# Kernel tuning notes

Measured on AMD Instinct MI355X. Metric: run time of the kernel, lower is better.

The kernel has to match this reference:

```python
import jax, jax.numpy as jnp
import numpy as np

N = 100000
E = 1600000
IN = 256
H = 4
F = 64
NEG_SLOPE = 0.05


def setup_inputs() -> dict:
    key = jax.random.key(0)
    ks = jax.random.split(key, 8)
    feat = jax.random.normal(ks[0], (N, IN), dtype=jnp.float32)
    src = jax.random.randint(ks[1], (E,), 0, N, dtype=jnp.int64)
    dst = jax.random.randint(ks[2], (E,), 0, N, dtype=jnp.int64)
    W_fc = jax.random.normal(ks[3], (H * F, IN), dtype=jnp.float32) * (2.0 / np.sqrt(IN + H * F))
    attn_l = jax.random.normal(ks[4], (H, F), dtype=jnp.float32) * 0.1
    attn_r = jax.random.normal(ks[5], (H, F), dtype=jnp.float32) * 0.1
    W_res = jax.random.normal(ks[6], (H * F, IN), dtype=jnp.float32) * (2.0 / np.sqrt(IN + H * F))
    bias = jnp.zeros((H * F,), dtype=jnp.float32)
    return {"feat": feat, "src": src, "dst": dst, "W_fc": W_fc,
            "attn_l": attn_l, "attn_r": attn_r, "W_res": W_res, "bias": bias}


def _leaky_relu(x):
    return jnp.where(x > 0, x, NEG_SLOPE * x)


def reference(feat, src, dst, W_fc, attn_l, attn_r, W_res, bias):
    # project: [N, H, F]
    feat_src = (feat @ W_fc.T).reshape(N, H, F)
    # attention logits per node: el/er [N, H]
    el = jnp.einsum('nhf,hf->nh', feat_src, attn_l)
    er = jnp.einsum('nhf,hf->nh', feat_src, attn_r)
    # edge SDDMM (u_add_v) + leaky_relu: [E, H]
    e = _leaky_relu(el[src] + er[dst])
    # edge softmax grouped by destination node
    emax = jax.ops.segment_max(e, dst, num_segments=N)          # [N, H]
    emax = jnp.where(jnp.isfinite(emax), emax, 0.0)             # empty segments
    ex = jnp.exp(e - emax[dst])                                 # [E, H]
    esum = jax.ops.segment_sum(ex, dst, num_segments=N)         # [N, H]
    a = ex / jnp.maximum(esum[dst], 1e-20)                      # [E, H]
    # u_mul_e + sum aggregation (SpMM): [N, H, F]
    msgs = feat_src[src] * a[:, :, None]                        # [E, H, F]
    rst = jax.ops.segment_sum(msgs, dst, num_segments=N)
    # residual + bias
    rst = rst + (feat @ W_res.T).reshape(N, H, F)
    rst = rst + bias.reshape(1, H, F)
    return rst, a
```

## Files before the change

### kernel.cpp

```cpp
#include <hip/hip_runtime.h>

#define NNODES 100000
#define NEDGES 1600000
#define KDIM 256
#define CDIM 256
#define NHEAD 4
#define FDIM 64
#define NEG 0.05f

typedef short bf16x8 __attribute__((ext_vector_type(8)));
typedef float f32x4  __attribute__((ext_vector_type(4)));
typedef __attribute__((address_space(3))) void*       lds_vp;
typedef __attribute__((address_space(1))) const void* glb_cvp;

__device__ __forceinline__ unsigned short f2b(float x) {
    unsigned int u = __float_as_uint(x);
    return (unsigned short)((u + 0x7FFFu + ((u >> 16) & 1u)) >> 16);
}
__device__ __forceinline__ float b2f(unsigned short b) {
    return __uint_as_float(((unsigned int)b) << 16);
}
__device__ __forceinline__ float lrelu(float x) { return x > 0.f ? x : NEG * x; }

__device__ __forceinline__ unsigned int fmap(float f) {
    unsigned int u = __float_as_uint(f);
    return u ^ ((u >> 31) ? 0xFFFFFFFFu : 0x80000000u);
}
__device__ __forceinline__ float funmap(unsigned int u) {
    return __uint_as_float(u ^ ((u & 0x80000000u) ? 0x80000000u : 0xFFFFFFFFu));
}

__global__ __launch_bounds__(256) void cvt_feat_count(
    const float* __restrict__ in, unsigned short* __restrict__ out,
    const int* __restrict__ dst, int* __restrict__ cnt)
{
    int i = (blockIdx.x * 256 + threadIdx.x) * 4;
    float4 v = *(const float4*)(in + i);
    ushort4 o;
    o.x = f2b(v.x); o.y = f2b(v.y); o.z = f2b(v.z); o.w = f2b(v.w);
    *(ushort4*)(out + i) = o;
    if (blockIdx.x < NEDGES / 256) {
        int e = blockIdx.x * 256 + threadIdx.x;
        atomicAdd(&cnt[dst[e]], 1);
    }
}

__global__ __launch_bounds__(256) void cvt_w(const float* __restrict__ Wfc,
                                             const float* __restrict__ Wres,
                                             unsigned short* __restrict__ out)
{
    int i = (blockIdx.x * 256 + threadIdx.x) * 4;
    float4 v = (i < 65536) ? *(const float4*)(Wfc + i)
                           : *(const float4*)(Wres + (i - 65536));
    ushort4 o;
    o.x = f2b(v.x); o.y = f2b(v.y); o.z = f2b(v.z); o.w = f2b(v.w);
    *(ushort4*)(out + i) = o;
}

__global__ __launch_bounds__(256) void gemm_mfma(
    const unsigned short* __restrict__ featb,
    const unsigned short* __restrict__ Wb,
    const float* __restrict__ bias,
    const float* __restrict__ attn_l, const float* __restrict__ attn_r,
    unsigned short* __restrict__ fsb,
    float* __restrict__ rst,
    float* __restrict__ el, float* __restrict__ er)
{
    const int b = blockIdx.x;
    const int grp = b >> 5, w32 = b & 31;
    const int bx = grp * 8 + (w32 & 7);
    const int ny = w32 >> 3;
    if (bx >= (NNODES + 127) / 128) return;

    __shared__ __align__(16) char smem[32768];
    char* sA = smem;
    char* sB = smem + 16384;

    const int tid = threadIdx.x;
    const int w = tid >> 6, l = tid & 63;
    const int wm = w & 1, wn = w >> 1;
    const int row0 = bx * 128;

    f32x4 acc[4][4];
#pragma unroll
    for (int tm = 0; tm < 4; ++tm)
#pragma unroll
        for (int tn = 0; tn < 4; ++tn) acc[tm][tn] = (f32x4)0.f;

    const int srow = tid >> 3;
    const int sslot = tid & 7;

    for (int k0 = 0; k0 < 256; k0 += 64) {
        if (k0) __syncthreads();
#pragma unroll
        for (int it = 0; it < 4; ++it) {
            int r = srow + it * 32;
            int gr = row0 + r; if (gr >= NNODES) gr = NNODES - 1;
            int kc = sslot ^ (r & 7);
            const unsigned short* g = featb + (size_t)gr * 256 + k0 + kc * 8;
            void* sp = sA + (it * 256 + w * 64) * 16;
            __builtin_amdgcn_global_load_lds((glb_cvp)g, (lds_vp)sp, 16, 0, 0);
        }
#pragma unroll
        for (int it = 0; it < 4; ++it) {
            int r = srow + it * 32;
            int kc = sslot ^ (r & 7);
            const unsigned short* g = Wb + (size_t)(ny * 128 + r) * 256 + k0 + kc * 8;
            void* sp = sB + (it * 256 + w * 64) * 16;
            __builtin_amdgcn_global_load_lds((glb_cvp)g, (lds_vp)sp, 16, 0, 0);
        }
        __syncthreads();

        const int quad = l >> 4;
#pragma unroll
        for (int kk = 0; kk < 2; ++kk) {
            const int kc = kk * 4 + quad;
            bf16x8 af[4], bq[4];
#pragma unroll
            for (int tm = 0; tm < 4; ++tm) {
                int m = wm * 64 + tm * 16 + (l & 15);
                af[tm] = *(const bf16x8*)(sA + m * 128 + ((kc ^ (m & 7)) * 16));
            }
#pragma unroll
            for (int tn = 0; tn < 4; ++tn) {
                int n = wn * 64 + tn * 16 + (l & 15);
                bq[tn] = *(const bf16x8*)(sB + n * 128 + ((kc ^ (n & 7)) * 16));
            }
#pragma unroll
            for (int tm = 0; tm < 4; ++tm)
#pragma unroll
                for (int tn = 0; tn < 4; ++tn)
                    acc[tm][tn] = __builtin_amdgcn_mfma_f32_16x16x32_bf16(
                        af[tm], bq[tn], acc[tm][tn], 0, 0, 0);
        }
    }

    const int quad = l >> 4, c15 = l & 15;
    if (ny < 2) {
#pragma unroll
        for (int tm = 0; tm < 4; ++tm) {
            int rb = row0 + wm * 64 + tm * 16 + quad * 4;
#pragma unroll
            for (int tn = 0; tn < 4; ++tn) {
                int cg = ny * 128 + wn * 64 + tn * 16 + c15;
#pragma unroll
                for (int reg = 0; reg < 4; ++reg) {
                    int r = rb + reg;
                    if (r < NNODES) fsb[(size_t)r * 256 + cg] = f2b(acc[tm][tn][reg]);
                }
            }
        }
        const int hh = ny * 2 + wn;
        float alv[4], arv[4];
#pragma unroll
        for (int tn = 0; tn < 4; ++tn) {
            alv[tn] = attn_l[hh * 64 + tn * 16 + c15];
            arv[tn] = attn_r[hh * 64 + tn * 16 + c15];
        }
#pragma unroll
        for (int tm = 0; tm < 4; ++tm) {
#pragma unroll
            for (int reg = 0; reg < 4; ++reg) {
                float pl = 0.f, pr = 0.f;
#pragma unroll
                for (int tn = 0; tn < 4; ++tn) {
                    float v = acc[tm][tn][reg];
                    pl = fmaf(v, alv[tn], pl);
                    pr = fmaf(v, arv[tn], pr);
                }
#pragma unroll
                for (int d = 1; d < 16; d <<= 1) {
                    pl += __shfl_xor(pl, d);
                    pr += __shfl_xor(pr, d);
                }
                if (c15 == 0) {
                    int r = row0 + wm * 64 + tm * 16 + quad * 4 + reg;
                    if (r < NNODES) {
                        el[r * NHEAD + hh] = pl;
                        er[r * NHEAD + hh] = pr;
                    }
                }
            }
        }
    } else {
#pragma unroll
        for (int tm = 0; tm < 4; ++tm) {
            int rb = row0 + wm * 64 + tm * 16 + quad * 4;
#pragma unroll
            for (int tn = 0; tn < 4; ++tn) {
                int co = (ny - 2) * 128 + wn * 64 + tn * 16 + c15;
                float b2 = bias[co];
#pragma unroll
                for (int reg = 0; reg < 4; ++reg) {
                    int r = rb + reg;
                    if (r < NNODES) rst[(size_t)r * 256 + co] = acc[tm][tn][reg] + b2;
                }
            }
        }
    }
}

__global__ __launch_bounds__(256) void gmax_kernel(const float* __restrict__ el,
                                                   unsigned int* __restrict__ gmax)
{
    int t = blockIdx.x * 256 + threadIdx.x;
    float4 mx = make_float4(-1e30f, -1e30f, -1e30f, -1e30f);
    for (int n = t; n < NNODES; n += 64 * 256) {
        float4 v = *(const float4*)(el + (size_t)n * 4);
        mx.x = fmaxf(mx.x, v.x); mx.y = fmaxf(mx.y, v.y);
        mx.z = fmaxf(mx.z, v.z); mx.w = fmaxf(mx.w, v.w);
    }
#pragma unroll
    for (int d = 32; d > 0; d >>= 1) {
        mx.x = fmaxf(mx.x, __shfl_xor(mx.x, d));
        mx.y = fmaxf(mx.y, __shfl_xor(mx.y, d));
        mx.z = fmaxf(mx.z, __shfl_xor(mx.z, d));
        mx.w = fmaxf(mx.w, __shfl_xor(mx.w, d));
    }
    if ((threadIdx.x & 63) == 0) {
        atomicMax(&gmax[0], fmap(mx.x));
        atomicMax(&gmax[1], fmap(mx.y));
        atomicMax(&gmax[2], fmap(mx.z));
        atomicMax(&gmax[3], fmap(mx.w));
    }
}

__global__ __launch_bounds__(256) void offset_kernel(const int* __restrict__ cnt,
                                                     int* __restrict__ off,
                                                     int* __restrict__ cursor,
                                                     int* __restrict__ total)
{
    int n = blockIdx.x * 256 + threadIdx.x;
    int lane = threadIdx.x & 63;
    int c = (n < NNODES) ? cnt[n] : 0;
    int incl = c;
#pragma unroll
    for (int d = 1; d < 64; d <<= 1) {
        int t = __shfl_up(incl, d);
        if (lane >= d) incl += t;
    }
    int wsum = __shfl(incl, 63);
    int base = 0;
    if (lane == 0) base = atomicAdd(total, wsum);
    base = __shfl(base, 0);
    if (n < NNODES) {
        int o = base + incl - c;
        off[n] = o;
        cursor[n] = o;
    }
}

__global__ __launch_bounds__(256) void scatter_kernel(const int* __restrict__ dst,
                                                      const int* __restrict__ src,
                                                      int* __restrict__ cursor,
                                                      int2* __restrict__ eperm)
{
    int e = blockIdx.x * 256 + threadIdx.x;
    if (e < NEDGES) {
        int s = src[e];
        int p = atomicAdd(&cursor[dst[e]], 1);
        eperm[p] = make_int2(e, s);
    }
}

__global__ __launch_bounds__(256) void agg_kernel(
    const int2* __restrict__ eperm,
    const int* __restrict__ off, const int* __restrict__ cnt,
    const float* __restrict__ el, const float* __restrict__ er,
    const unsigned int* __restrict__ gmax,
    const unsigned short* __restrict__ fsb,
    float* __restrict__ rst,
    float* __restrict__ a_out)
{
    const int tid = threadIdx.x;
    const int wv = tid >> 6, lane = tid & 63;
    const int n = blockIdx.x * 4 + wv;
    const int deg = cnt[n];
    if (deg == 0) return;
    const int o0 = off[n];

    __shared__ __align__(16) float a_sh[4][64][4];
    float* aw = &a_sh[wv][0][0];

    const float4 er4 = *(const float4*)(er + (size_t)n * NHEAD);
    const uint4 g4 = *(const uint4*)gmax;
    float4 M;
    M.x = lrelu(funmap(g4.x) + er4.x);
    M.y = lrelu(funmap(g4.y) + er4.y);
    M.z = lrelu(funmap(g4.z) + er4.z);
    M.w = lrelu(funmap(g4.w) + er4.w);

    float4 s = make_float4(0.f, 0.f, 0.f, 0.f);
    int s0_save = 0, e0_save = 0;
    float4 l0_save = make_float4(0.f, 0.f, 0.f, 0.f);

    for (int base = 0; base < deg; base += 64) {
        int i = base + lane;
        bool valid = i < deg;
        int2 es = eperm[o0 + (valid ? i : deg - 1)];
        int sidx = es.y;
        float4 ev = *(const float4*)(el + (size_t)sidx * NHEAD);
        float4 l;
        l.x = lrelu(ev.x + er4.x); l.y = lrelu(ev.y + er4.y);
        l.z = lrelu(ev.z + er4.z); l.w = lrelu(ev.w + er4.w);
        if (base == 0) { s0_save = sidx; e0_save = es.x; l0_save = l; }
        s.x += valid ? __expf(l.x - M.x) : 0.f;
        s.y += valid ? __expf(l.y - M.y) : 0.f;
        s.z += valid ? __expf(l.z - M.z) : 0.f;
        s.w += valid ? __expf(l.w - M.w) : 0.f;
    }
#pragma unroll
    for (int d = 32; d > 0; d >>= 1) {
        s.x += __shfl_xor(s.x, d);
        s.y += __shfl_xor(s.y, d);
        s.z += __shfl_xor(s.z, d);
        s.w += __shfl_xor(s.w, d);
    }
    float4 inv;
    inv.x = 1.f / fmaxf(s.x, 1e-20f);
    inv.y = 1.f / fmaxf(s.y, 1e-20f);
    inv.z = 1.f / fmaxf(s.z, 1e-20f);
    inv.w = 1.f / fmaxf(s.w, 1e-20f);

    const int rsel = lane >> 5;
    const int c    = lane & 31;
    const int h2   = c >> 3;
    const unsigned int coff = (unsigned)c << 4;

    float acc[8];
#pragma unroll
    for (int k = 0; k < 8; ++k) acc[k] = 0.f;

    for (int base = 0; base < deg; base += 64) {
        int i = base + lane;
        bool valid = i < deg;
        int sidx, e; float4 l;
        if (base == 0) { sidx = s0_save; e = e0_save; l = l0_save; }
        else {
            int2 es = eperm[o0 + (valid ? i : deg - 1)];
            e = es.x; sidx = es.y;
            float4 ev = *(const float4*)(el + (size_t)sidx * NHEAD);
            l.x = lrelu(ev.x + er4.x); l.y = lrelu(ev.y + er4.y);
            l.z = lrelu(ev.z + er4.z); l.w = lrelu(ev.w + er4.w);
        }
        float4 a;
        a.x = valid ? __expf(l.x - M.x) * inv.x : 0.f;
        a.y = valid ? __expf(l.y - M.y) * inv.y : 0.f;
        a.z = valid ? __expf(l.z - M.z) * inv.z : 0.f;
        a.w = valid ? __expf(l.w - M.w) * inv.w : 0.f;
        *(float4*)(aw + (lane << 2)) = a;

        if (valid) *(float4*)(a_out + (size_t)e * NHEAD) = a;

        int nc = min(64, deg - base);
#pragma unroll 8
        for (int jj = 0; jj < nc; jj += 2) {
            int sjA = __builtin_amdgcn_readlane(sidx, jj);
            int sjB = __builtin_amdgcn_readlane(sidx, jj + 1);
            float av = aw[((jj + rsel) << 2) + h2];
            int sj = rsel ? sjB : sjA;
            unsigned int boff = ((unsigned)sj << 9) + coff;
            uint4 p = *(const uint4*)((const char*)fsb + boff);
            acc[0] = fmaf(av, __uint_as_float(p.x << 16),         acc[0]);
            acc[1] = fmaf(av, __uint_as_float(p.x & 0xffff0000u), acc[1]);
            acc[2] = fmaf(av, __uint_as_float(p.y << 16),         acc[2]);
            acc[3] = fmaf(av, __uint_as_float(p.y & 0xffff0000u), acc[3]);
            acc[4] = fmaf(av, __uint_as_float(p.z << 16),         acc[4]);
            acc[5] = fmaf(av, __uint_as_float(p.z & 0xffff0000u), acc[5]);
            acc[6] = fmaf(av, __uint_as_float(p.w << 16),         acc[6]);
            acc[7] = fmaf(av, __uint_as_float(p.w & 0xffff0000u), acc[7]);
        }
    }
#pragma unroll
    for (int k = 0; k < 8; ++k) acc[k] += __shfl_xor(acc[k], 32);
    float o0v = rsel ? acc[4] : acc[0];
    float o1v = rsel ? acc[5] : acc[1];
    float o2v = rsel ? acc[6] : acc[2];
    float o3v = rsel ? acc[7] : acc[3];
    size_t ro = (size_t)n * 256 + ((size_t)c << 3) + ((size_t)rsel << 2);
    float4 r = *(float4*)(rst + ro);
    r.x += o0v; r.y += o1v; r.z += o2v; r.w += o3v;
    *(float4*)(rst + ro) = r;
}

extern "C" void kernel_launch(void* const* d_in, const int* in_sizes, int n_in,
                              void* d_out, int out_size, void* d_ws, size_t ws_size,
                              hipStream_t stream) {
    const float* feat   = (const float*)d_in[0];
    const int*   src    = (const int*)d_in[1];
    const int*   dst    = (const int*)d_in[2];
    const float* Wfc    = (const float*)d_in[3];
    const float* attn_l = (const float*)d_in[4];
    const float* attn_r = (const float*)d_in[5];
    const float* Wres   = (const float*)d_in[6];
    const float* bias   = (const float*)d_in[7];

    float* rst   = (float*)d_out;
    float* a_out = (float*)d_out + (size_t)NNODES * CDIM;

    unsigned short* featb = (unsigned short*)d_ws;
    unsigned short* fsb   = featb + (size_t)NNODES * CDIM;
    unsigned short* Wb    = fsb + (size_t)NNODES * CDIM;
    float* el      = (float*)(Wb + 512 * 256);
    float* er      = el + (size_t)NNODES * NHEAD;
    unsigned int* gmax = (unsigned int*)(er + (size_t)NNODES * NHEAD);
    int* cnt    = (int*)(gmax + 4);
    int* off    = cnt + NNODES;
    int* cursor = off + NNODES;
    int* total  = cursor + NNODES;
    int2* eperm = (int2*)featb;

    hipMemsetAsync(cnt, 0, NNODES * sizeof(int), stream);
    hipMemsetAsync(total, 0, 4 * sizeof(int), stream);
    hipMemsetAsync(gmax, 0, 4 * sizeof(unsigned int), stream);

    cvt_feat_count<<<(NNODES * CDIM) / (256 * 4), 256, 0, stream>>>(feat, featb,
                                                                    dst, cnt);
    cvt_w<<<(512 * 256) / (256 * 4), 256, 0, stream>>>(Wfc, Wres, Wb);

    gemm_mfma<<<3136, 256, 0, stream>>>(featb, Wb, bias, attn_l, attn_r,
                                        fsb, rst, el, er);

    gmax_kernel<<<64, 256, 0, stream>>>(el, gmax);

    offset_kernel<<<(NNODES + 255) / 256, 256, 0, stream>>>(cnt, off, cursor, total);
    scatter_kernel<<<(NEDGES + 255) / 256, 256, 0, stream>>>(dst, src, cursor,
                                                             eperm);

    agg_kernel<<<NNODES / 4, 256, 0, stream>>>(eperm, off, cnt, el, er, gmax,
                                               fsb, rst, a_out);
}
```

Before: 625.6 us.

## Transpose MFMA output for vectorized epilogue stores and fuse gmax into offset kernel

Swaps the MFMA operand order so each lane holds four consecutive columns of one row. The epilogue can then write packed bf16 (uint2) and float4 stores instead of scattered scalar stores, and the el/er reductions need only two cross-quad shuffles. The global el max reduction moves into offset_kernel, which removes one launch, and the three memsets become two. The trade-off is more atomics on gmax, one set per wave across the whole grid.

Result: slower. 676.7 us (+8.2%).

```diff
diff --git a/kernel.cpp b/kernel.cpp
--- a/kernel.cpp
+++ b/kernel.cpp
@@ -131,104 +131,78 @@
 #pragma unroll
                 for (int tn = 0; tn < 4; ++tn)
                     acc[tm][tn] = __builtin_amdgcn_mfma_f32_16x16x32_bf16(
-                        af[tm], bq[tn], acc[tm][tn], 0, 0, 0);
+                        bq[tn], af[tm], acc[tm][tn], 0, 0, 0);
         }
     }
 
     const int quad = l >> 4, c15 = l & 15;
     if (ny < 2) {
+        const int hh = ny * 2 + wn;
+        float4 alv[4], arv[4];
+#pragma unroll
+        for (int tn = 0; tn < 4; ++tn) {
+            alv[tn] = *(const float4*)(attn_l + hh * 64 + tn * 16 + quad * 4);
+            arv[tn] = *(const float4*)(attn_r + hh * 64 + tn * 16 + quad * 4);
+        }
 #pragma unroll
         for (int tm = 0; tm < 4; ++tm) {
-            int rb = row0 + wm * 64 + tm * 16 + quad * 4;
+            int row = row0 + wm * 64 + tm * 16 + c15;
+            bool ok = row < NNODES;
 #pragma unroll
             for (int tn = 0; tn < 4; ++tn) {
-                int cg = ny * 128 + wn * 64 + tn * 16 + c15;
+                int cb = ny * 128 + wn * 64 + tn * 16 + quad * 4;
+                unsigned int lo = (unsigned int)f2b(acc[tm][tn][0])
+                                | ((unsigned int)f2b(acc[tm][tn][1]) << 16);
+                unsigned int hi = (unsigned int)f2b(acc[tm][tn][2])
+                                | ((unsigned int)f2b(acc[tm][tn][3]) << 16);
+                if (ok) *(uint2*)(fsb + (size_t)row * 256 + cb) = make_uint2(lo, hi);
+            }
+            float pl = 0.f, pr = 0.f;
+#pragma unroll
+            for (int tn = 0; tn < 4; ++tn) {
 #pragma unroll
                 for (int reg = 0; reg < 4; ++reg) {
-                    int r = rb + reg;
-                    if (r < NNODES) fsb[(size_t)r * 256 + cg] = f2b(acc[tm][tn][reg]);
+                    float v = acc[tm][tn][reg];
+                    pl = fmaf(v, ((const float*)&alv[tn])[reg], pl);
+                    pr = fmaf(v, ((const float*)&arv[tn])[reg], pr);
                 }
             }
-        }
-        const int hh = ny * 2 + wn;
-        float alv[4], arv[4];
-#pragma unroll
-        for (int tn = 0; tn < 4; ++tn) {
-            alv[tn] = attn_l[hh * 64 + tn * 16 + c15];
-            arv[tn] = attn_r[hh * 64 + tn * 16 + c15];
-        }
+            pl += __shfl_xor(pl, 16); pl += __shfl_xor(pl, 32);
+            pr += __shfl_xor(pr, 16); pr += __shfl_xor(pr, 32);
+            if (quad == 0 && ok) {
+                el[row * NHEAD + hh] = pl;
+                er[row * NHEAD + hh] = pr;
+            }
+        }
+    } else {
+        float4 b4[4];
+#pragma unroll
+        for (int tn = 0; tn < 4; ++tn)
+            b4[tn] = *(const float4*)(bias + (ny - 2) * 128 + wn * 64 + tn * 16 + quad * 4);
 #pragma unroll
         for (int tm = 0; tm < 4; ++tm) {
-#pragma unroll
-            for (int reg = 0; reg < 4; ++reg) {
-                float pl = 0.f, pr = 0.f;
-#pragma unroll
-                for (int tn = 0; tn < 4; ++tn) {
-                    float v = acc[tm][tn][reg];
-                    pl = fmaf(v, alv[tn], pl);
-                    pr = fmaf(v, arv[tn], pr);
-                }
-#pragma unroll
-                for (int d = 1; d < 16; d <<= 1) {
-                    pl += __shfl_xor(pl, d);
-                    pr += __shfl_xor(pr, d);
-                }
-                if (c15 == 0) {
-                    int r = row0 + wm * 64 + tm * 16 + quad * 4 + reg;
-                    if (r < NNODES) {
-                        el[r * NHEAD + hh] = pl;
-                        er[r * NHEAD + hh] = pr;
-                    }
-                }
-            }
-        }
-    } else {
-#pragma unroll
-        for (int tm = 0; tm < 4; ++tm) {
-            int rb = row0 + wm * 64 + tm * 16 + quad * 4;
+            int row = row0 + wm * 64 + tm * 16 + c15;
+            if (row >= NNODES) continue;
 #pragma unroll
             for (int tn = 0; tn < 4; ++tn) {
-                int co = (ny - 2) * 128 + wn * 64 + tn * 16 + c15;
-                float b2 = bias[co];
-#pragma unroll
-                for (int reg = 0; reg < 4; ++reg) {
-                    int r = rb + reg;
-                    if (r < NNODES) rst[(size_t)r * 256 + co] = acc[tm][tn][reg] + b2;
-                }
-            }
-        }
-    }
-}
-
-__global__ __launch_bounds__(256) void gmax_kernel(const float* __restrict__ el,
-                                                   unsigned int* __restrict__ gmax)
-{
-    int t = blockIdx.x * 256 + threadIdx.x;
-    float4 mx = make_float4(-1e30f, -1e30f, -1e30f, -1e30f);
-    for (int n = t; n < NNODES; n += 64 * 256) {
-        float4 v = *(const float4*)(el + (size_t)n * 4);
-        mx.x = fmaxf(mx.x, v.x); mx.y = fmaxf(mx.y, v.y);
-        mx.z = fmaxf(mx.z, v.z); mx.w = fmaxf(mx.w, v.w);
-    }
-#pragma unroll
-    for (int d = 32; d > 0; d >>= 1) {
-        mx.x = fmaxf(mx.x, __shfl_xor(mx.x, d));
-        mx.y = fmaxf(mx.y, __shfl_xor(mx.y, d));
-        mx.z = fmaxf(mx.z, __shfl_xor(mx.z, d));
-        mx.w = fmaxf(mx.w, __shfl_xor(mx.w, d));
-    }
-    if ((threadIdx.x & 63) == 0) {
-        atomicMax(&gmax[0], fmap(mx.x));
-        atomicMax(&gmax[1], fmap(mx.y));
-        atomicMax(&gmax[2], fmap(mx.z));
-        atomicMax(&gmax[3], fmap(mx.w));
+                int cb = (ny - 2) * 128 + wn * 64 + tn * 16 + quad * 4;
+                float4 o;
+                o.x = acc[tm][tn][0] + b4[tn].x;
+                o.y = acc[tm][tn][1] + b4[tn].y;
+                o.z = acc[tm][tn][2] + b4[tn].z;
+                o.w = acc[tm][tn][3] + b4[tn].w;
+                *(float4*)(rst + (size_t)row * 256 + cb) = o;
+            }
+        }
     }
 }
 
 __global__ __launch_bounds__(256) void offset_kernel(const int* __restrict__ cnt,
                                                      int* __restrict__ off,
                                                      int* __restrict__ cursor,
-                                                     int* __restrict__ total)
+                                                     int* __restrict__ total,
+                                                     const float* __restrict__ el,
+                                                     unsigned int* __restrict__ gmax)
 {
     int n = blockIdx.x * 256 + threadIdx.x;
     int lane = threadIdx.x & 63;
@@ -247,6 +221,21 @@
         int o = base + incl - c;
         off[n] = o;
         cursor[n] = o;
+    }
+    float4 mx = make_float4(-1e30f, -1e30f, -1e30f, -1e30f);
+    if (n < NNODES) mx = *(const float4*)(el + (size_t)n * 4);
+#pragma unroll
+    for (int d = 32; d > 0; d >>= 1) {
+        mx.x = fmaxf(mx.x, __shfl_xor(mx.x, d));
+        mx.y = fmaxf(mx.y, __shfl_xor(mx.y, d));
+        mx.z = fmaxf(mx.z, __shfl_xor(mx.z, d));
+        mx.w = fmaxf(mx.w, __shfl_xor(mx.w, d));
+    }
+    if (lane == 0) {
+        atomicMax(&gmax[0], fmap(mx.x));
+        atomicMax(&gmax[1], fmap(mx.y));
+        atomicMax(&gmax[2], fmap(mx.z));
+        atomicMax(&gmax[3], fmap(mx.w));
     }
 }
 
@@ -404,15 +393,14 @@
     float* el      = (float*)(Wb + 512 * 256);
     float* er      = el + (size_t)NNODES * NHEAD;
     unsigned int* gmax = (unsigned int*)(er + (size_t)NNODES * NHEAD);
-    int* cnt    = (int*)(gmax + 4);
+    int* total  = (int*)(gmax + 4);
+    int* cnt    = total + 4;
     int* off    = cnt + NNODES;
     int* cursor = off + NNODES;
-    int* total  = cursor + NNODES;
     int2* eperm = (int2*)featb;
 
+    hipMemsetAsync(gmax, 0, 8 * sizeof(int), stream);
     hipMemsetAsync(cnt, 0, NNODES * sizeof(int), stream);
-    hipMemsetAsync(total, 0, 4 * sizeof(int), stream);
-    hipMemsetAsync(gmax, 0, 4 * sizeof(unsigned int), stream);
 
     cvt_feat_count<<<(NNODES * CDIM) / (256 * 4), 256, 0, stream>>>(feat, featb,
                                                                     dst, cnt);
@@ -421,9 +409,8 @@
     gemm_mfma<<<3136, 256, 0, stream>>>(featb, Wb, bias, attn_l, attn_r,
                                         fsb, rst, el, er);
 
-    gmax_kernel<<<64, 256, 0, stream>>>(el, gmax);
-
-    offset_kernel<<<(NNODES + 255) / 256, 256, 0, stream>>>(cnt, off, cursor, total);
+    offset_kernel<<<(NNODES + 255) / 256, 256, 0, stream>>>(cnt, off, cursor,
+                                                            total, el, gmax);
     scatter_kernel<<<(NEDGES + 255) / 256, 256, 0, stream>>>(dst, src, cursor,
                                                              eperm);
 
```
